# Performance work log

Measured on AMD Instinct MI355X. Metric: run time of the kernel, lower is better.

The kernel has to match this reference:

```python
import jax, jax.numpy as jnp
import numpy as np

V, EMB, H, N, E, B = 100000, 300, 64, 20000, 160000, 4096
L, T = 2, 3  # layer_timesteps = [3, 3]


def setup_inputs() -> dict:
    key = jax.random.key(0)
    ks = jax.random.split(key, 24)
    ri = lambda k, shape, hi: jax.random.randint(k, shape, 0, hi)
    rn = lambda k, shape, s=0.05: (jax.random.normal(k, shape, dtype=jnp.float32) * s)
    emb_table = rn(ks[7], (V, EMB), 0.1).at[0].set(0.0)  # padding_idx=0 row is zeros
    return {
        'emb_ind0': ri(ks[0], (N,), V),
        'emb_ind1': ri(ks[1], (N,), V),
        'adj0': ri(ks[2], (E, 2), N),
        'adj1': ri(ks[3], (E, 2), N),
        'prop_ind0': ri(ks[4], (B,), N),
        'prop_ind1': ri(ks[5], (B,), N),
        'labels': ri(ks[6], (B,), 2),
        'emb_table': emb_table,
        'proj_W': rn(ks[8], (EMB, H)),   # emb_proj weight (stored input-major)
        'proj_b': jnp.zeros((H,), jnp.float32),
        'msg_W': rn(ks[9], (L, H, H)),   # per-layer edge-type-0 message linear
        'msg_b': jnp.zeros((L, H), jnp.float32),
        'gru_Wih': rn(ks[10], (L, 3 * H, H)),
        'gru_Whh': rn(ks[11], (L, 3 * H, H)),
        'gru_bih': jnp.zeros((L, 3 * H), jnp.float32),
        'gru_bhh': jnp.zeros((L, 3 * H), jnp.float32),
        'cla_W1': rn(ks[12], (2 * H, 16)),
        'cla_b1': jnp.zeros((16,), jnp.float32),
        'cla_W2': rn(ks[13], (16, 1)),
        'cla_b2': jnp.zeros((1,), jnp.float32),
    }


def _gru_cell(x, h, Wih, Whh, bih, bhh):
    # torch.nn.GRUCell math
    gi = x @ Wih.T + bih
    gh = h @ Whh.T + bhh
    i_r, i_z, i_n = jnp.split(gi, 3, axis=-1)
    h_r, h_z, h_n = jnp.split(gh, 3, axis=-1)
    r = jax.nn.sigmoid(i_r + h_r)
    z = jax.nn.sigmoid(i_z + h_z)
    n = jnp.tanh(i_n + r * h_n)
    return (1.0 - z) * n + z * h


def reference(emb_ind0, emb_ind1, adj0, adj1, prop_ind0, prop_ind1, labels,
              emb_table, proj_W, proj_b, msg_W, msg_b,
              gru_Wih, gru_Whh, gru_bih, gru_bhh,
              cla_W1, cla_b1, cla_W2, cla_b2):
    def ggnn(x, adj):
        src, tgt = adj[:, 0], adj[:, 1]
        h = x
        for l in range(L):              # 2 structurally distinct layers
            for _ in range(T):          # 3 timesteps each
                m = h[src] @ msg_W[l] + msg_b[l]                     # [E, H] gather + transform
                inc = jax.ops.segment_sum(m, tgt, num_segments=N)    # scatter-add messages
                h = _gru_cell(inc, h, gru_Wih[l], gru_Whh[l], gru_bih[l], gru_bhh[l])
        return h

    def branch(emb_ind, adj, prop_ind):
        ge = emb_table[emb_ind]          # embedding lookup [N, EMB]
        ge = ge @ proj_W + proj_b        # emb_proj -> [N, H]
        ge = ggnn(ge, adj)
        return ge[prop_ind]              # index_select -> [B, H]

    g0 = branch(emb_ind0, adj0, prop_ind0)
    g1 = branch(emb_ind1, adj1, prop_ind1)
    ge = jnp.concatenate([g0, g1], axis=-1)                 # match='concat' -> [B, 2H]
    hid = jax.nn.relu(ge @ cla_W1 + cla_b1)
    logits = jax.nn.sigmoid(hid @ cla_W2 + cla_b2)          # [B, 1], num_class=1 path
    p = logits.squeeze(-1)
    y = labels.astype(p.dtype)
    eps = 1e-7  # mirrors torch BCELoss log-clamping
    loss = -jnp.mean(y * jnp.log(jnp.clip(p, eps, 1.0))
                     + (1.0 - y) * jnp.log(jnp.clip(1.0 - p, eps, 1.0)))
    return logits, loss
```

## Files before the change

kernel.cpp:

```cpp
#include <hip/hip_runtime.h>
#include <hip/hip_bf16.h>

typedef unsigned short u16;
typedef __attribute__((ext_vector_type(8))) short s16x8;
typedef __attribute__((ext_vector_type(4))) float f32x4;

#define NN 20000
#define HH 64
#define EMBD 300
#define EE 160000
#define BB 4096
#define NODES 40000
#define SLST  640000

#define OFF_PROJB 0
#define OFF_MSGB  64
#define OFF_BIH   192
#define OFF_BHH   576
#define OFF_CW1T  960
#define OFF_CB1   3008
#define OFF_CW2   3024
#define OFF_CB2   3040
#define PARAM_SZ  3072

#define PB_WIH   0
#define PB_WHH   24576
#define PB_WMT   49152
#define PB_PROJT 57344
#define PB_SZ    77824

#define APAD 344

__device__ __forceinline__ float b2f(u16 u) {
    union { unsigned int i; float f; } v; v.i = ((unsigned int)u) << 16; return v.f;
}
__device__ __forceinline__ u16 f2b(float f) {
    union { float f; unsigned int u; } v; v.f = f;
    unsigned int u = v.u;
    return (u16)((u + 0x7FFFu + ((u >> 16) & 1u)) >> 16);
}
__device__ __forceinline__ float ldf(const void* p, long long i, int isbf) {
    return isbf ? b2f(((const u16*)p)[i]) : ((const float*)p)[i];
}
__device__ __forceinline__ u16 ldb(const void* p, long long i, int isbf) {
    return isbf ? ((const u16*)p)[i] : f2b(((const float*)p)[i]);
}
__device__ __forceinline__ void stf(void* p, long long i, int isbf, float v) {
    if (isbf) ((u16*)p)[i] = f2b(v);
    else      ((float*)p)[i] = v;
}

__global__ void sniff_kernel(const u16* probe, int* flag)
{
    if (threadIdx.x == 0 && blockIdx.x == 0) {
        int good = 0;
        for (int i = 0; i < 128; i += 2) {
            unsigned int e = (probe[i] >> 7) & 0xFF;
            if (e >= 105 && e <= 127) good++;
        }
        *flag = (good >= 48) ? 1 : 0;
    }
}

__global__ __launch_bounds__(256) void conv_kernel(
    const void* projW, const void* projb, const void* msgW, const void* msgb,
    const void* wih, const void* whh, const void* bih, const void* bhh,
    const void* cw1, const void* cb1, const void* cw2, const void* cb2,
    float* P, u16* PB, const int* flag)
{
    int isbf = *flag;
    int i = blockIdx.x * 256 + threadIdx.x;
    if (i < 64)    P[OFF_PROJB + i] = ldf(projb, i, isbf);
    if (i < 128)   P[OFF_MSGB + i]  = ldf(msgb, i, isbf);
    if (i < 384)   { P[OFF_BIH + i] = ldf(bih, i, isbf); P[OFF_BHH + i] = ldf(bhh, i, isbf); }
    if (i < 2048)  { int t = i >> 7, k = i & 127; P[OFF_CW1T + i] = ldf(cw1, (long long)k * 16 + t, isbf); }
    if (i < 16)    { P[OFF_CB1 + i] = ldf(cb1, i, isbf); P[OFF_CW2 + i] = ldf(cw2, i, isbf); }
    if (i == 0)    P[OFF_CB2] = ldf(cb2, 0, isbf);

    if (i < 24576) {
        int l = i / 12288, r = i - l * 12288;
        int frag = r >> 9, rr = r & 511, lane = rr >> 3, e = rr & 7;
        int jt = frag >> 1, kt = frag & 1;
        int srow = jt * 16 + (lane & 15);
        int sk = kt * 32 + ((lane >> 4) << 3) + e;
        long long si = (long long)l * 12288 + srow * 64 + sk;
        PB[PB_WIH + i] = ldb(wih, si, isbf);
        PB[PB_WHH + i] = ldb(whh, si, isbf);
    }
    if (i < 8192) {
        int l = i >> 12, r = i & 4095;
        int frag = r >> 9, rr = r & 511, lane = rr >> 3, e = rr & 7;
        int jt = frag >> 1, kt = frag & 1;
        int srow = jt * 16 + (lane & 15);
        int sk = kt * 32 + ((lane >> 4) << 3) + e;
        PB[PB_WMT + i] = ldb(msgW, (long long)l * 4096 + sk * 64 + srow, isbf);
    }
    if (i < 20480) {
        int frag = i >> 9, rr = i & 511, lane = rr >> 3, e = rr & 7;
        int jt = frag / 10, kt = frag - jt * 10;
        int srow = jt * 16 + (lane & 15);
        int sk = kt * 32 + ((lane >> 4) << 3) + e;
        PB[PB_PROJT + i] = (sk < 300) ? ldb(projW, (long long)sk * 64 + srow, isbf) : (u16)0;
    }
}

__global__ __launch_bounds__(256) void hist_kernel(const int* __restrict__ adj0,
                                                   const int* __restrict__ adj1, int* off)
{
    int e = blockIdx.x * 256 + threadIdx.x;
    if (e >= 2 * EE) return;
    int b = e / EE, le = e - b * EE;
    const int* adj = b ? adj1 : adj0;
    int tgt = adj[2 * le + 1];
    atomicAdd(&off[b * (NN + 1) + tgt + 1], 1);
}

__global__ __launch_bounds__(1024) void scan_kernel(int* off, int* cursor)
{
    int b = blockIdx.x;
    int* o = off + (size_t)b * (NN + 1);
    int* cur = cursor + (size_t)b * NN;
    __shared__ int wsum[16];
    __shared__ int wscan[16];
    int tid = threadIdx.x, wv = tid >> 6, lane = tid & 63;
    int base = 0;
    for (int start = 0; start < NN; start += 1024) {
        int i = start + tid;
        int v = (i < NN) ? o[i + 1] : 0;
        int orig = v;
        #pragma unroll
        for (int d = 1; d < 64; d <<= 1) {
            int t = __shfl_up(v, d);
            if (lane >= d) v += t;
        }
        if (lane == 63) wsum[wv] = v;
        __syncthreads();
        if (tid < 16) {
            int w = wsum[tid];
            #pragma unroll
            for (int d = 1; d < 16; d <<= 1) {
                int t = __shfl_up(w, d, 16);
                if (tid >= d) w += t;
            }
            wscan[tid] = w;
        }
        __syncthreads();
        int woff = (wv == 0) ? 0 : wscan[wv - 1];
        int excl = base + woff + v - orig;
        if (i < NN) { o[i] = excl; cur[i] = excl; }
        base += wscan[15];
    }
    if (tid == 0) o[NN] = base;
}

__global__ __launch_bounds__(256) void scatter_kernel(const int* __restrict__ adj0,
                                                      const int* __restrict__ adj1,
                                                      int* cursor, int* esrc)
{
    int e = blockIdx.x * 256 + threadIdx.x;
    if (e >= 2 * EE) return;
    int b = e / EE, le = e - b * EE;
    const int* adj = b ? adj1 : adj0;
    int src = adj[2 * le + 0];
    int tgt = adj[2 * le + 1];
    int pos = atomicAdd(&cursor[b * NN + tgt], 1);
    esrc[(size_t)b * EE + pos] = src;
}

__global__ __launch_bounds__(256) void projm_kernel(const void* emb,
                                                    const int* __restrict__ i0,
                                                    const int* __restrict__ i1,
                                                    const float* __restrict__ P,
                                                    const u16* __restrict__ PB,
                                                    u16* __restrict__ h, const int* flag)
{
    __shared__ u16 sA[64 * APAD];
    int isbf = *flag;
    int tid = threadIdx.x;
    int node0 = blockIdx.x * 64;

    {
        int r = tid >> 2, sub = tid & 3;
        int n = node0 + r;
        int b = n >= NN;
        int ln = n - b * NN;
        int idx = b ? i1[ln] : i0[ln];
        if (isbf) {
            const ushort4* src = (const ushort4*)((const u16*)emb + (size_t)idx * EMBD);
            ushort4* dst = (ushort4*)(sA + r * APAD);
            for (int c = sub; c < 75; c += 4) dst[c] = src[c];
            if (sub == 0) {
                ushort4 z = {0, 0, 0, 0};
                for (int c = 75; c < 80; ++c) dst[c] = z;
            }
        } else {
            const float* src = (const float*)emb + (size_t)idx * EMBD;
            for (int k = sub; k < 300; k += 4) sA[r * APAD + k] = f2b(src[k]);
            if (sub == 0) for (int k = 300; k < 320; ++k) sA[r * APAD + k] = 0;
        }
    }

    int wv = tid >> 6, lane = tid & 63, quad = lane >> 4, cn = lane & 15;
    int m0 = wv * 16;
    f32x4 acc[4];
    #pragma unroll
    for (int j = 0; j < 4; ++j) {
        float bb = P[OFF_PROJB + j * 16 + cn];
        acc[j] = {bb, bb, bb, bb};
    }
    #pragma unroll
    for (int kt = 0; kt < 10; ++kt) {
        s16x8 a = *(const s16x8*)&sA[(m0 + cn) * APAD + kt * 32 + quad * 8];
        #pragma unroll
        for (int j = 0; j < 4; ++j) {
            s16x8 bfr = *(const s16x8*)&PB[PB_PROJT + (j * 10 + kt) * 512 + lane * 8];
            acc[j] = __builtin_amdgcn_mfma_f32_16x16x32_bf16(a, bfr, acc[j], 0, 0, 0);
        }
    }
    #pragma unroll
    for (int j = 0; j < 4; ++j)
        #pragma unroll
        for (int r = 0; r < 4; ++r)
            h[(size_t)j * SLST + (size_t)(node0 + m0 + quad * 4 + r) * 16 + cn] = f2b(acc[j][r]);
}

__global__ __launch_bounds__(256) void gatherS_kernel(const u16* __restrict__ h_old,
                                                      u16* __restrict__ Sbuf,
                                                      const int* __restrict__ ioff,
                                                      const int* __restrict__ esrc)
{
    int b = blockIdx.x;
    int slice = b & 3;
    int tile = b >> 2;
    int tid = threadIdx.x;
    int i = tid >> 4, feat = tid & 15;
    int node = tile * 16 + i;
    int br = node >= NN;
    int ln = node - br * NN;
    const int* o = ioff + (size_t)br * (NN + 1);
    int s0 = o[ln], s1 = o[ln + 1];
    const int* es = esrc + (size_t)br * EE;
    const u16* hb = h_old + (size_t)slice * SLST + (size_t)br * NN * 16;
    float a0 = 0.f, a1 = 0.f, a2 = 0.f, a3 = 0.f;
    int e = s0;
    for (; e + 4 <= s1; e += 4) {
        int e0 = es[e], e1 = es[e + 1], e2 = es[e + 2], e3 = es[e + 3];
        a0 += b2f(hb[(size_t)e0 * 16 + feat]);
        a1 += b2f(hb[(size_t)e1 * 16 + feat]);
        a2 += b2f(hb[(size_t)e2 * 16 + feat]);
        a3 += b2f(hb[(size_t)e3 * 16 + feat]);
    }
    for (; e < s1; ++e) a0 += b2f(hb[(size_t)es[e] * 16 + feat]);
    Sbuf[(size_t)slice * SLST + (size_t)node * 16 + feat] = f2b(a0 + a1 + a2 + a3);
}

__global__ __launch_bounds__(256) void gstep_kernel(const u16* __restrict__ Sbuf,
                                                    const u16* __restrict__ h_old,
                                                    u16* __restrict__ h_new,
                                                    const int* __restrict__ ioff,
                                                    const float* __restrict__ P,
                                                    const u16* __restrict__ PB, int l)
{
    __shared__ u16 s_S[4096];
    __shared__ u16 s_h[4096];
    __shared__ float s_deg[64];

    int tid = threadIdx.x;
    int wv = tid >> 6, lane = tid & 63;
    int node0 = blockIdx.x * 64;
    int m0 = wv * 16;

    #pragma unroll
    for (int it = 0; it < 2; ++it) {
        int idx = it * 64 + lane;
        int slice = idx >> 5;
        int rem = idx & 31;
        int nlo = rem >> 1, half = rem & 1;
        int row = m0 + nlo;
        size_t goff = (size_t)slice * SLST + (size_t)(node0 + row) * 16 + half * 8;
        *(uint4*)(s_h + row * 64 + slice * 16 + half * 8) = *(const uint4*)(h_old + goff);
        *(uint4*)(s_S + row * 64 + slice * 16 + half * 8) = *(const uint4*)(Sbuf + goff);
    }
    if (lane < 16) {
        int row = m0 + lane;
        int n = node0 + row;
        int br = n >= NN;
        int ln = n - br * NN;
        const int* o = ioff + (size_t)br * (NN + 1);
        s_deg[row] = (float)(o[ln + 1] - o[ln]);
    }

    int quad = lane >> 4, cn = lane & 15;
    int arow = (m0 + cn) * 64 + quad * 8;
    int fl = lane * 8;

    s16x8 aS0 = *(const s16x8*)&s_S[arow];
    s16x8 aS1 = *(const s16x8*)&s_S[arow + 32];
    const u16* WM = PB + PB_WMT + (size_t)l * 4096;
    #pragma unroll
    for (int jt = 0; jt < 4; ++jt) {
        float mb = P[OFF_MSGB + l * 64 + jt * 16 + cn];
        f32x4 acc;
        acc[0] = s_deg[m0 + quad * 4 + 0] * mb;
        acc[1] = s_deg[m0 + quad * 4 + 1] * mb;
        acc[2] = s_deg[m0 + quad * 4 + 2] * mb;
        acc[3] = s_deg[m0 + quad * 4 + 3] * mb;
        acc = __builtin_amdgcn_mfma_f32_16x16x32_bf16(aS0, *(const s16x8*)&WM[(jt * 2 + 0) * 512 + fl], acc, 0, 0, 0);
        acc = __builtin_amdgcn_mfma_f32_16x16x32_bf16(aS1, *(const s16x8*)&WM[(jt * 2 + 1) * 512 + fl], acc, 0, 0, 0);
        #pragma unroll
        for (int r = 0; r < 4; ++r)
            s_S[(m0 + quad * 4 + r) * 64 + jt * 16 + cn] = f2b(acc[r]);
    }

    s16x8 aI0 = *(const s16x8*)&s_S[arow];
    s16x8 aI1 = *(const s16x8*)&s_S[arow + 32];
    s16x8 aH0 = *(const s16x8*)&s_h[arow];
    s16x8 aH1 = *(const s16x8*)&s_h[arow + 32];
    const u16* WI = PB + PB_WIH + (size_t)l * 12288;
    const u16* WH = PB + PB_WHH + (size_t)l * 12288;
    const float* bi = P + OFF_BIH + l * 192;
    const float* bh = P + OFF_BHH + l * 192;

    #pragma unroll
    for (int c = 0; c < 4; ++c) {
        int j0 = c * 16;
        float vr = bi[j0 + cn], vz = bi[64 + j0 + cn], vn = bi[128 + j0 + cn];
        float wr = bh[j0 + cn], wz = bh[64 + j0 + cn], wn = bh[128 + j0 + cn];
        f32x4 gr = {vr, vr, vr, vr}, gz = {vz, vz, vz, vz}, gn = {vn, vn, vn, vn};
        f32x4 hr = {wr, wr, wr, wr}, hz = {wz, wz, wz, wz}, hn = {wn, wn, wn, wn};
        int fr = (c * 2) * 512 + fl, frz = ((4 + c) * 2) * 512 + fl, frn = ((8 + c) * 2) * 512 + fl;
        gr = __builtin_amdgcn_mfma_f32_16x16x32_bf16(aI0, *(const s16x8*)&WI[fr], gr, 0, 0, 0);
        gr = __builtin_amdgcn_mfma_f32_16x16x32_bf16(aI1, *(const s16x8*)&WI[fr + 512], gr, 0, 0, 0);
        gz = __builtin_amdgcn_mfma_f32_16x16x32_bf16(aI0, *(const s16x8*)&WI[frz], gz, 0, 0, 0);
        gz = __builtin_amdgcn_mfma_f32_16x16x32_bf16(aI1, *(const s16x8*)&WI[frz + 512], gz, 0, 0, 0);
        gn = __builtin_amdgcn_mfma_f32_16x16x32_bf16(aI0, *(const s16x8*)&WI[frn], gn, 0, 0, 0);
        gn = __builtin_amdgcn_mfma_f32_16x16x32_bf16(aI1, *(const s16x8*)&WI[frn + 512], gn, 0, 0, 0);
        hr = __builtin_amdgcn_mfma_f32_16x16x32_bf16(aH0, *(const s16x8*)&WH[fr], hr, 0, 0, 0);
        hr = __builtin_amdgcn_mfma_f32_16x16x32_bf16(aH1, *(const s16x8*)&WH[fr + 512], hr, 0, 0, 0);
        hz = __builtin_amdgcn_mfma_f32_16x16x32_bf16(aH0, *(const s16x8*)&WH[frz], hz, 0, 0, 0);
        hz = __builtin_amdgcn_mfma_f32_16x16x32_bf16(aH1, *(const s16x8*)&WH[frz + 512], hz, 0, 0, 0);
        hn = __builtin_amdgcn_mfma_f32_16x16x32_bf16(aH0, *(const s16x8*)&WH[frn], hn, 0, 0, 0);
        hn = __builtin_amdgcn_mfma_f32_16x16x32_bf16(aH1, *(const s16x8*)&WH[frn + 512], hn, 0, 0, 0);
        #pragma unroll
        for (int r = 0; r < 4; ++r) {
            int row = m0 + quad * 4 + r;
            float rr = 1.f / (1.f + __expf(-(gr[r] + hr[r])));
            float zz = 1.f / (1.f + __expf(-(gz[r] + hz[r])));
            float nn = tanhf(gn[r] + rr * hn[r]);
            float ho = b2f(s_h[row * 64 + j0 + cn]);
            h_new[(size_t)c * SLST + (size_t)(node0 + row) * 16 + cn] = f2b((1.f - zz) * nn + zz * ho);
        }
    }
}

__global__ __launch_bounds__(256) void cls_kernel(const u16* __restrict__ h,
                                                  const int* __restrict__ p0,
                                                  const int* __restrict__ p1,
                                                  const int* __restrict__ labels,
                                                  const float* __restrict__ P,
                                                  void* out, float* partial, const int* flag)
{
    int isbf = *flag;
    int wv = threadIdx.x >> 6, lane = threadIdx.x & 63;
    int s = blockIdx.x * 4 + wv;
    int n0 = p0[s], n1 = p1[s];
    size_t sl = (size_t)(lane >> 4) * SLST;
    float f0 = b2f(h[sl + (size_t)n0 * 16 + (lane & 15)]);
    float f1 = b2f(h[sl + (size_t)(NN + n1) * 16 + (lane & 15)]);
    float z = P[OFF_CB2];
    #pragma unroll
    for (int t = 0; t < 16; ++t) {
        float part = f0 * P[OFF_CW1T + t * 128 + lane] + f1 * P[OFF_CW1T + t * 128 + 64 + lane];
        #pragma unroll
        for (int off = 32; off; off >>= 1) part += __shfl_xor(part, off);
        z += fmaxf(part + P[OFF_CB1 + t], 0.f) * P[OFF_CW2 + t];
    }
    float p = 1.f / (1.f + expf(-z));
    float y = (float)labels[s];
    const float eps = 1e-7f;
    float pc  = fminf(fmaxf(p, eps), 1.f);
    float pc1 = fminf(fmaxf(1.f - p, eps), 1.f);
    float term = y * logf(pc) + (1.f - y) * logf(pc1);
    __shared__ float red[4];
    if (lane == 0) { stf(out, s, isbf, p); red[wv] = term; }
    __syncthreads();
    if (threadIdx.x == 0) partial[blockIdx.x] = red[0] + red[1] + red[2] + red[3];
}

__global__ __launch_bounds__(256) void loss_kernel(const float* __restrict__ partial,
                                                   void* out, const int* flag)
{
    __shared__ float red[256];
    int tid = threadIdx.x;
    float s = 0.f;
    for (int i = tid; i < 1024; i += 256) s += partial[i];
    red[tid] = s;
    __syncthreads();
    for (int d = 128; d > 0; d >>= 1) {
        if (tid < d) red[tid] += red[tid + d];
        __syncthreads();
    }
    if (tid == 0) stf(out, BB, *flag, -red[0] / (float)BB);
}

extern "C" void kernel_launch(void* const* d_in, const int* in_sizes, int n_in,
                              void* d_out, int out_size, void* d_ws, size_t ws_size,
                              hipStream_t stream)
{
    const int* adj0   = (const int*)d_in[2];
    const int* adj1   = (const int*)d_in[3];
    const int* prop0  = (const int*)d_in[4];
    const int* prop1  = (const int*)d_in[5];
    const int* labels = (const int*)d_in[6];

    int* flag = (int*)d_ws;
    float* P  = (float*)d_ws + 16;
    u16* PB   = (u16*)(P + PARAM_SZ);
    u16* h0   = PB + PB_SZ;
    u16* h1   = h0 + (size_t)4 * SLST / 4 * 4;
    u16* SB   = h1 + (size_t)2560000;
    float* partial = (float*)(SB + (size_t)2560000);
    int* ioff   = (int*)(partial + 1024);
    int* cursor = ioff + 2 * (NN + 1) + 62;
    int* esrc   = cursor + 2 * NN;

    hipMemsetAsync(ioff, 0, 2 * (NN + 1) * sizeof(int), stream);

    sniff_kernel<<<1, 64, 0, stream>>>((const u16*)d_in[8], flag);
    conv_kernel<<<96, 256, 0, stream>>>(d_in[8], d_in[9], d_in[10], d_in[11], d_in[12], d_in[13],
                                        d_in[14], d_in[15], d_in[16], d_in[17], d_in[18], d_in[19],
                                        P, PB, flag);
    hist_kernel<<<(2 * EE) / 256, 256, 0, stream>>>(adj0, adj1, ioff);
    scan_kernel<<<2, 1024, 0, stream>>>(ioff, cursor);
    scatter_kernel<<<(2 * EE) / 256, 256, 0, stream>>>(adj0, adj1, cursor, esrc);
    projm_kernel<<<(2 * NN) / 64, 256, 0, stream>>>(d_in[7], (const int*)d_in[0],
                                                    (const int*)d_in[1], P, PB, h0, flag);

    u16* hcur = h0;
    u16* hnext = h1;
    for (int l = 0; l < 2; ++l) {
        for (int t = 0; t < 3; ++t) {
            gatherS_kernel<<<4 * (NODES / 16), 256, 0, stream>>>(hcur, SB, ioff, esrc);
            gstep_kernel<<<NODES / 64, 256, 0, stream>>>(SB, hcur, hnext, ioff, P, PB, l);
            u16* tmp = hcur; hcur = hnext; hnext = tmp;
        }
    }

    cls_kernel<<<BB / 4, 256, 0, stream>>>(hcur, prop0, prop1, labels, P, d_out, partial, flag);
    loss_kernel<<<1, 256, 0, stream>>>(partial, d_out, flag);
}
```

Baseline: 463.4 us.

## Switch hidden state to two 32-feature slices and shuffle-broadcast edge indices

New measurement: 444.4 us. 4.1% less time.

```diff
diff --git a/kernel.cpp b/kernel.cpp
--- a/kernel.cpp
+++ b/kernel.cpp
@@ -11,7 +11,7 @@
 #define EE 160000
 #define BB 4096
 #define NODES 40000
-#define SLST  640000
+#define SL32  1280000
 
 #define OFF_PROJB 0
 #define OFF_MSGB  64
@@ -221,7 +221,7 @@
     for (int j = 0; j < 4; ++j)
         #pragma unroll
         for (int r = 0; r < 4; ++r)
-            h[(size_t)j * SLST + (size_t)(node0 + m0 + quad * 4 + r) * 16 + cn] = f2b(acc[j][r]);
+            h[(size_t)(j >> 1) * SL32 + (size_t)(node0 + m0 + quad * 4 + r) * 32 + (j & 1) * 16 + cn] = f2b(acc[j][r]);
 }
 
 __global__ __launch_bounds__(256) void gatherS_kernel(const u16* __restrict__ h_old,
@@ -230,28 +230,42 @@
                                                       const int* __restrict__ esrc)
 {
     int b = blockIdx.x;
-    int slice = b & 3;
-    int tile = b >> 2;
+    int slice = b & 1;
+    int tile = b >> 1;
     int tid = threadIdx.x;
-    int i = tid >> 4, feat = tid & 15;
-    int node = tile * 16 + i;
+    int i = tid >> 5, feat = tid & 31;
+    int node = tile * 8 + i;
     int br = node >= NN;
     int ln = node - br * NN;
     const int* o = ioff + (size_t)br * (NN + 1);
     int s0 = o[ln], s1 = o[ln + 1];
     const int* es = esrc + (size_t)br * EE;
-    const u16* hb = h_old + (size_t)slice * SLST + (size_t)br * NN * 16;
+    const u16* hb = h_old + (size_t)slice * SL32 + (size_t)br * NN * 32;
     float a0 = 0.f, a1 = 0.f, a2 = 0.f, a3 = 0.f;
-    int e = s0;
-    for (; e + 4 <= s1; e += 4) {
-        int e0 = es[e], e1 = es[e + 1], e2 = es[e + 2], e3 = es[e + 3];
-        a0 += b2f(hb[(size_t)e0 * 16 + feat]);
-        a1 += b2f(hb[(size_t)e1 * 16 + feat]);
-        a2 += b2f(hb[(size_t)e2 * 16 + feat]);
-        a3 += b2f(hb[(size_t)e3 * 16 + feat]);
-    }
-    for (; e < s1; ++e) a0 += b2f(hb[(size_t)es[e] * 16 + feat]);
-    Sbuf[(size_t)slice * SLST + (size_t)node * 16 + feat] = f2b(a0 + a1 + a2 + a3);
+    int base = s0;
+    int rem = s1 - s0;
+    while (rem > 0) {
+        int cnt = rem < 32 ? rem : 32;
+        int myidx = (feat < cnt) ? es[base + feat] : 0;
+        int j = 0;
+        for (; j + 4 <= cnt; j += 4) {
+            int e0 = __shfl(myidx, j, 32);
+            int e1 = __shfl(myidx, j + 1, 32);
+            int e2 = __shfl(myidx, j + 2, 32);
+            int e3 = __shfl(myidx, j + 3, 32);
+            a0 += b2f(hb[(size_t)e0 * 32 + feat]);
+            a1 += b2f(hb[(size_t)e1 * 32 + feat]);
+            a2 += b2f(hb[(size_t)e2 * 32 + feat]);
+            a3 += b2f(hb[(size_t)e3 * 32 + feat]);
+        }
+        for (; j < cnt; ++j) {
+            int e0 = __shfl(myidx, j, 32);
+            a0 += b2f(hb[(size_t)e0 * 32 + feat]);
+        }
+        base += cnt;
+        rem -= cnt;
+    }
+    Sbuf[(size_t)slice * SL32 + (size_t)node * 32 + feat] = f2b(a0 + a1 + a2 + a3);
 }
 
 __global__ __launch_bounds__(256) void gstep_kernel(const u16* __restrict__ Sbuf,
@@ -273,13 +287,12 @@
     #pragma unroll
     for (int it = 0; it < 2; ++it) {
         int idx = it * 64 + lane;
-        int slice = idx >> 5;
-        int rem = idx & 31;
-        int nlo = rem >> 1, half = rem & 1;
+        int c = idx & 7;
+        int nlo = idx >> 3;
         int row = m0 + nlo;
-        size_t goff = (size_t)slice * SLST + (size_t)(node0 + row) * 16 + half * 8;
-        *(uint4*)(s_h + row * 64 + slice * 16 + half * 8) = *(const uint4*)(h_old + goff);
-        *(uint4*)(s_S + row * 64 + slice * 16 + half * 8) = *(const uint4*)(Sbuf + goff);
+        size_t goff = (size_t)(c >> 2) * SL32 + (size_t)(node0 + row) * 32 + (c & 3) * 8;
+        *(uint4*)(s_h + row * 64 + c * 8) = *(const uint4*)(h_old + goff);
+        *(uint4*)(s_S + row * 64 + c * 8) = *(const uint4*)(Sbuf + goff);
     }
     if (lane < 16) {
         int row = m0 + lane;
@@ -348,7 +361,7 @@
             float zz = 1.f / (1.f + __expf(-(gz[r] + hz[r])));
             float nn = tanhf(gn[r] + rr * hn[r]);
             float ho = b2f(s_h[row * 64 + j0 + cn]);
-            h_new[(size_t)c * SLST + (size_t)(node0 + row) * 16 + cn] = f2b((1.f - zz) * nn + zz * ho);
+            h_new[(size_t)(c >> 1) * SL32 + (size_t)(node0 + row) * 32 + (c & 1) * 16 + cn] = f2b((1.f - zz) * nn + zz * ho);
         }
     }
 }
@@ -364,9 +377,10 @@
     int wv = threadIdx.x >> 6, lane = threadIdx.x & 63;
     int s = blockIdx.x * 4 + wv;
     int n0 = p0[s], n1 = p1[s];
-    size_t sl = (size_t)(lane >> 4) * SLST;
-    float f0 = b2f(h[sl + (size_t)n0 * 16 + (lane & 15)]);
-    float f1 = b2f(h[sl + (size_t)(NN + n1) * 16 + (lane & 15)]);
+    size_t sl = (size_t)(lane >> 5) * SL32;
+    int fo = lane & 31;
+    float f0 = b2f(h[sl + (size_t)n0 * 32 + fo]);
+    float f1 = b2f(h[sl + (size_t)(NN + n1) * 32 + fo]);
     float z = P[OFF_CB2];
     #pragma unroll
     for (int t = 0; t < 16; ++t) {
@@ -417,9 +431,9 @@
     float* P  = (float*)d_ws + 16;
     u16* PB   = (u16*)(P + PARAM_SZ);
     u16* h0   = PB + PB_SZ;
-    u16* h1   = h0 + (size_t)4 * SLST / 4 * 4;
-    u16* SB   = h1 + (size_t)2560000;
-    float* partial = (float*)(SB + (size_t)2560000);
+    u16* h1   = h0 + (size_t)2 * SL32;
+    u16* SB   = h1 + (size_t)2 * SL32;
+    float* partial = (float*)(SB + (size_t)2 * SL32);
     int* ioff   = (int*)(partial + 1024);
     int* cursor = ioff + 2 * (NN + 1) + 62;
     int* esrc   = cursor + 2 * NN;
@@ -440,7 +454,7 @@
     u16* hnext = h1;
     for (int l = 0; l < 2; ++l) {
         for (int t = 0; t < 3; ++t) {
-            gatherS_kernel<<<4 * (NODES / 16), 256, 0, stream>>>(hcur, SB, ioff, esrc);
+            gatherS_kernel<<<2 * (NODES / 8), 256, 0, stream>>>(hcur, SB, ioff, esrc);
             gstep_kernel<<<NODES / 64, 256, 0, stream>>>(SB, hcur, hnext, ioff, P, PB, l);
             u16* tmp = hcur; hcur = hnext; hnext = tmp;
         }
```

## Fuse neighbor gather into GRU step kernel with row-major node layout

Applied to the files above, without the earlier changes.

Result: faster. 397.7 us (-14.2%).

```diff
diff --git a/kernel.cpp b/kernel.cpp
--- a/kernel.cpp
+++ b/kernel.cpp
@@ -11,7 +11,6 @@
 #define EE 160000
 #define BB 4096
 #define NODES 40000
-#define SLST  640000
 
 #define OFF_PROJB 0
 #define OFF_MSGB  64
@@ -221,84 +220,86 @@
     for (int j = 0; j < 4; ++j)
         #pragma unroll
         for (int r = 0; r < 4; ++r)
-            h[(size_t)j * SLST + (size_t)(node0 + m0 + quad * 4 + r) * 16 + cn] = f2b(acc[j][r]);
-}
-
-__global__ __launch_bounds__(256) void gatherS_kernel(const u16* __restrict__ h_old,
-                                                      u16* __restrict__ Sbuf,
-                                                      const int* __restrict__ ioff,
-                                                      const int* __restrict__ esrc)
-{
-    int b = blockIdx.x;
-    int slice = b & 3;
-    int tile = b >> 2;
-    int tid = threadIdx.x;
-    int i = tid >> 4, feat = tid & 15;
-    int node = tile * 16 + i;
-    int br = node >= NN;
-    int ln = node - br * NN;
-    const int* o = ioff + (size_t)br * (NN + 1);
-    int s0 = o[ln], s1 = o[ln + 1];
-    const int* es = esrc + (size_t)br * EE;
-    const u16* hb = h_old + (size_t)slice * SLST + (size_t)br * NN * 16;
-    float a0 = 0.f, a1 = 0.f, a2 = 0.f, a3 = 0.f;
-    int e = s0;
-    for (; e + 4 <= s1; e += 4) {
-        int e0 = es[e], e1 = es[e + 1], e2 = es[e + 2], e3 = es[e + 3];
-        a0 += b2f(hb[(size_t)e0 * 16 + feat]);
-        a1 += b2f(hb[(size_t)e1 * 16 + feat]);
-        a2 += b2f(hb[(size_t)e2 * 16 + feat]);
-        a3 += b2f(hb[(size_t)e3 * 16 + feat]);
-    }
-    for (; e < s1; ++e) a0 += b2f(hb[(size_t)es[e] * 16 + feat]);
-    Sbuf[(size_t)slice * SLST + (size_t)node * 16 + feat] = f2b(a0 + a1 + a2 + a3);
-}
-
-__global__ __launch_bounds__(256) void gstep_kernel(const u16* __restrict__ Sbuf,
-                                                    const u16* __restrict__ h_old,
+            h[(size_t)(node0 + m0 + quad * 4 + r) * 64 + j * 16 + cn] = f2b(acc[j][r]);
+}
+
+__global__ __launch_bounds__(256) void fstep_kernel(const u16* __restrict__ h_old,
                                                     u16* __restrict__ h_new,
                                                     const int* __restrict__ ioff,
+                                                    const int* __restrict__ esrc,
                                                     const float* __restrict__ P,
                                                     const u16* __restrict__ PB, int l)
 {
-    __shared__ u16 s_S[4096];
-    __shared__ u16 s_h[4096];
-    __shared__ float s_deg[64];
+    __shared__ u16 s_S[32 * 64];
+    __shared__ u16 s_h[32 * 64];
+    __shared__ float s_deg[32];
 
     int tid = threadIdx.x;
+    int node0 = blockIdx.x * 32;
+
+    {
+        int team = tid >> 3, oct = tid & 7;
+        int node = node0 + team;
+        int br = node >= NN;
+        int ln = node - br * NN;
+        const int* o = ioff + (size_t)br * (NN + 1);
+        int s0 = o[ln], s1 = o[ln + 1];
+        const int* es = esrc + (size_t)br * EE;
+        const u16* hb = h_old + (size_t)br * NN * 64;
+
+        float acc[8];
+        #pragma unroll
+        for (int k = 0; k < 8; ++k) acc[k] = 0.f;
+
+        int base = s0, rem = s1 - s0;
+        while (rem > 0) {
+            int cnt = rem < 8 ? rem : 8;
+            int myidx = es[base + (oct < cnt ? oct : cnt - 1)];
+            #pragma unroll
+            for (int j = 0; j < 8; ++j) {
+                int e = __shfl(myidx, j, 8);
+                uint4 v = *(const uint4*)&hb[(size_t)e * 64 + oct * 8];
+                float w = (j < cnt) ? 1.f : 0.f;
+                #pragma unroll
+                for (int p = 0; p < 4; ++p) {
+                    unsigned int u = ((const unsigned int*)&v)[p];
+                    union { unsigned int i; float f; } lo, hi;
+                    lo.i = u << 16; hi.i = u & 0xffff0000u;
+                    acc[2 * p]     += w * lo.f;
+                    acc[2 * p + 1] += w * hi.f;
+                }
+            }
+            base += cnt;
+            rem -= cnt;
+        }
+
+        u16 pk[8];
+        #pragma unroll
+        for (int k = 0; k < 8; ++k) pk[k] = f2b(acc[k]);
+        *(uint4*)&s_S[team * 64 + oct * 8] = *(const uint4*)pk;
+        *(uint4*)&s_h[team * 64 + oct * 8] =
+            *(const uint4*)&h_old[(size_t)node * 64 + oct * 8];
+        if (oct == 0) s_deg[team] = (float)(s1 - s0);
+    }
+    __syncthreads();
+
     int wv = tid >> 6, lane = tid & 63;
-    int node0 = blockIdx.x * 64;
-    int m0 = wv * 16;
-
-    #pragma unroll
-    for (int it = 0; it < 2; ++it) {
-        int idx = it * 64 + lane;
-        int slice = idx >> 5;
-        int rem = idx & 31;
-        int nlo = rem >> 1, half = rem & 1;
-        int row = m0 + nlo;
-        size_t goff = (size_t)slice * SLST + (size_t)(node0 + row) * 16 + half * 8;
-        *(uint4*)(s_h + row * 64 + slice * 16 + half * 8) = *(const uint4*)(h_old + goff);
-        *(uint4*)(s_S + row * 64 + slice * 16 + half * 8) = *(const uint4*)(Sbuf + goff);
-    }
-    if (lane < 16) {
-        int row = m0 + lane;
-        int n = node0 + row;
-        int br = n >= NN;
-        int ln = n - br * NN;
-        const int* o = ioff + (size_t)br * (NN + 1);
-        s_deg[row] = (float)(o[ln + 1] - o[ln]);
-    }
-
+    int wr = wv >> 1, wc = wv & 1;
+    int m0 = wr * 16;
     int quad = lane >> 4, cn = lane & 15;
     int arow = (m0 + cn) * 64 + quad * 8;
     int fl = lane * 8;
 
     s16x8 aS0 = *(const s16x8*)&s_S[arow];
     s16x8 aS1 = *(const s16x8*)&s_S[arow + 32];
+    s16x8 aH0 = *(const s16x8*)&s_h[arow];
+    s16x8 aH1 = *(const s16x8*)&s_h[arow + 32];
+    __syncthreads();
+
     const u16* WM = PB + PB_WMT + (size_t)l * 4096;
     #pragma unroll
-    for (int jt = 0; jt < 4; ++jt) {
+    for (int jtl = 0; jtl < 2; ++jtl) {
+        int jt = wc * 2 + jtl;
         float mb = P[OFF_MSGB + l * 64 + jt * 16 + cn];
         f32x4 acc;
         acc[0] = s_deg[m0 + quad * 4 + 0] * mb;
@@ -311,24 +312,24 @@
         for (int r = 0; r < 4; ++r)
             s_S[(m0 + quad * 4 + r) * 64 + jt * 16 + cn] = f2b(acc[r]);
     }
+    __syncthreads();
 
     s16x8 aI0 = *(const s16x8*)&s_S[arow];
     s16x8 aI1 = *(const s16x8*)&s_S[arow + 32];
-    s16x8 aH0 = *(const s16x8*)&s_h[arow];
-    s16x8 aH1 = *(const s16x8*)&s_h[arow + 32];
     const u16* WI = PB + PB_WIH + (size_t)l * 12288;
     const u16* WH = PB + PB_WHH + (size_t)l * 12288;
     const float* bi = P + OFF_BIH + l * 192;
     const float* bh = P + OFF_BHH + l * 192;
 
     #pragma unroll
-    for (int c = 0; c < 4; ++c) {
-        int j0 = c * 16;
+    for (int cl = 0; cl < 2; ++cl) {
+        int jt = wc * 2 + cl;
+        int j0 = jt * 16;
         float vr = bi[j0 + cn], vz = bi[64 + j0 + cn], vn = bi[128 + j0 + cn];
-        float wr = bh[j0 + cn], wz = bh[64 + j0 + cn], wn = bh[128 + j0 + cn];
+        float wr_ = bh[j0 + cn], wz = bh[64 + j0 + cn], wn = bh[128 + j0 + cn];
         f32x4 gr = {vr, vr, vr, vr}, gz = {vz, vz, vz, vz}, gn = {vn, vn, vn, vn};
-        f32x4 hr = {wr, wr, wr, wr}, hz = {wz, wz, wz, wz}, hn = {wn, wn, wn, wn};
-        int fr = (c * 2) * 512 + fl, frz = ((4 + c) * 2) * 512 + fl, frn = ((8 + c) * 2) * 512 + fl;
+        f32x4 hr = {wr_, wr_, wr_, wr_}, hz = {wz, wz, wz, wz}, hn = {wn, wn, wn, wn};
+        int fr = (jt * 2) * 512 + fl, frz = ((4 + jt) * 2) * 512 + fl, frn = ((8 + jt) * 2) * 512 + fl;
         gr = __builtin_amdgcn_mfma_f32_16x16x32_bf16(aI0, *(const s16x8*)&WI[fr], gr, 0, 0, 0);
         gr = __builtin_amdgcn_mfma_f32_16x16x32_bf16(aI1, *(const s16x8*)&WI[fr + 512], gr, 0, 0, 0);
         gz = __builtin_amdgcn_mfma_f32_16x16x32_bf16(aI0, *(const s16x8*)&WI[frz], gz, 0, 0, 0);
@@ -348,7 +349,7 @@
             float zz = 1.f / (1.f + __expf(-(gz[r] + hz[r])));
             float nn = tanhf(gn[r] + rr * hn[r]);
             float ho = b2f(s_h[row * 64 + j0 + cn]);
-            h_new[(size_t)c * SLST + (size_t)(node0 + row) * 16 + cn] = f2b((1.f - zz) * nn + zz * ho);
+            h_new[(size_t)(node0 + row) * 64 + j0 + cn] = f2b((1.f - zz) * nn + zz * ho);
         }
     }
 }
@@ -364,9 +365,8 @@
     int wv = threadIdx.x >> 6, lane = threadIdx.x & 63;
     int s = blockIdx.x * 4 + wv;
     int n0 = p0[s], n1 = p1[s];
-    size_t sl = (size_t)(lane >> 4) * SLST;
-    float f0 = b2f(h[sl + (size_t)n0 * 16 + (lane & 15)]);
-    float f1 = b2f(h[sl + (size_t)(NN + n1) * 16 + (lane & 15)]);
+    float f0 = b2f(h[(size_t)n0 * 64 + lane]);
+    float f1 = b2f(h[(size_t)(NN + n1) * 64 + lane]);
     float z = P[OFF_CB2];
     #pragma unroll
     for (int t = 0; t < 16; ++t) {
@@ -417,9 +417,8 @@
     float* P  = (float*)d_ws + 16;
     u16* PB   = (u16*)(P + PARAM_SZ);
     u16* h0   = PB + PB_SZ;
-    u16* h1   = h0 + (size_t)4 * SLST / 4 * 4;
-    u16* SB   = h1 + (size_t)2560000;
-    float* partial = (float*)(SB + (size_t)2560000);
+    u16* h1   = h0 + (size_t)NODES * 64;
+    float* partial = (float*)(h1 + (size_t)NODES * 64);
     int* ioff   = (int*)(partial + 1024);
     int* cursor = ioff + 2 * (NN + 1) + 62;
     int* esrc   = cursor + 2 * NN;
@@ -440,8 +439,7 @@
     u16* hnext = h1;
     for (int l = 0; l < 2; ++l) {
         for (int t = 0; t < 3; ++t) {
-            gatherS_kernel<<<4 * (NODES / 16), 256, 0, stream>>>(hcur, SB, ioff, esrc);
-            gstep_kernel<<<NODES / 64, 256, 0, stream>>>(SB, hcur, hnext, ioff, P, PB, l);
+            fstep_kernel<<<NODES / 32, 256, 0, stream>>>(hcur, hnext, ioff, esrc, P, PB, l);
             u16* tmp = hcur; hcur = hnext; hnext = tmp;
         }
     }
```
